# Optimization experiments

Hardware: AMD Instinct MI355X
Metric: run time of the kernel (lower is better)

The kernel has to match this reference:

```python
import jax, jax.numpy as jnp
import numpy as np

EMBED_DIM = 1024
NUM_HEADS = 16
HEAD_DIM = EMBED_DIM // NUM_HEADS


def setup_inputs() -> dict:
    key = jax.random.key(0)
    ks = jax.random.split(key, 7)
    B, S, E = 2, 2048, EMBED_DIM
    s = 1.0 / np.sqrt(E)
    return {
        "x": jax.random.normal(ks[0], (B, S, E), dtype=jnp.float32),
        "W_qkv": jax.random.uniform(ks[1], (3 * E, E), jnp.float32, -s, s),
        "b_qkv": jax.random.uniform(ks[2], (3 * E,), jnp.float32, -s, s),
        "W_proj": jax.random.uniform(ks[3], (E, E), jnp.float32, -s, s),
        "b_proj": jax.random.uniform(ks[4], (E,), jnp.float32, -s, s),
        "gamma": jnp.ones((E,), jnp.float32),
        "beta": jnp.zeros((E,), jnp.float32),
    }


def reference(x, W_qkv, b_qkv, W_proj, b_proj, gamma, beta):
    B, S, E = x.shape
    H, D = NUM_HEADS, HEAD_DIM
    residual = x
    # fused QKV projection: [B,S,3E] -> [B,S,3,H,D]
    qkv = (jnp.einsum('bse,fe->bsf', x, W_qkv) + b_qkv).reshape(B, S, 3, H, D)
    q = qkv[:, :, 0].transpose(0, 2, 1, 3)  # [B,H,S,D]
    k = qkv[:, :, 1].transpose(0, 2, 1, 3)
    v = qkv[:, :, 2].transpose(0, 2, 1, 3)
    scale = 1.0 / jnp.sqrt(jnp.float32(D)).astype(x.dtype)
    attn = jnp.einsum('bhqd,bhkd->bhqk', q, k) * scale  # [B,H,S,S]
    attn = jax.nn.softmax(attn, axis=-1)
    out = jnp.einsum('bhqk,bhkd->bhqd', attn, v)  # [B,H,S,D]
    out = out.transpose(0, 2, 1, 3).reshape(B, S, E)
    out = jnp.einsum('bse,fe->bsf', out, W_proj) + b_proj
    # LayerNorm(out + residual), eps=1e-5 (torch default)
    y = out + residual
    mu = jnp.mean(y, axis=-1, keepdims=True)
    var = jnp.mean(jnp.square(y - mu), axis=-1, keepdims=True)
    return (y - mu) * jax.lax.rsqrt(var + 1e-5) * gamma + beta
```

## Files before the change

kernel.cpp:

```cpp
#include <hip/hip_runtime.h>
#include <cstdint>

#define EDIM 1024
#define NHEADS 16
#define HDIM 64
#define BATCH 2
#define SEQ 2048
#define MROWS (BATCH * SEQ)

typedef __attribute__((ext_vector_type(8))) short bf16x8;
typedef __attribute__((ext_vector_type(4))) float f32x4;

__device__ __forceinline__ unsigned short f2bf(float f) {
  union { float f; unsigned u; } v; v.f = f;
  unsigned r = v.u + 0x7FFFu + ((v.u >> 16) & 1u);
  return (unsigned short)(r >> 16);
}

__device__ __forceinline__ unsigned cvt_pk_bf16(float lo, float hi) {
  unsigned r;
  asm("v_cvt_pk_bf16_f32 %0, %1, %2" : "=v"(r) : "v"(lo), "v"(hi));
  return r;
}

__device__ __forceinline__ void gload16(const void* g, void* l) {
  __builtin_amdgcn_global_load_lds(
      (const __attribute__((address_space(1))) unsigned int*)g,
      (__attribute__((address_space(3))) unsigned int*)l, 16, 0, 0);
}

__global__ __launch_bounds__(256) void cvt_kernel(const float* __restrict__ in,
                                                  unsigned short* __restrict__ out,
                                                  int n) {
  const int i = (blockIdx.x * 256 + threadIdx.x) * 8;
  if (i >= n) return;
  const float4 a = *(const float4*)&in[i];
  const float4 b = *(const float4*)&in[i + 4];
  unsigned short u[8];
  u[0] = f2bf(a.x); u[1] = f2bf(a.y); u[2] = f2bf(a.z); u[3] = f2bf(a.w);
  u[4] = f2bf(b.x); u[5] = f2bf(b.y); u[6] = f2bf(b.z); u[7] = f2bf(b.w);
  *(uint4*)&out[i] = *(uint4*)u;
}

template <int MODE>
__global__ __launch_bounds__(256) void gemm_bf16(
    const unsigned short* __restrict__ A, const unsigned short* __restrict__ Bw,
    const float* __restrict__ bias, const float* __restrict__ resid,
    unsigned short* __restrict__ q_out, unsigned short* __restrict__ k_out,
    unsigned short* __restrict__ v_out, float* __restrict__ y_out,
    int M, int N, int K) {
  __shared__ unsigned short As[128 * 64];
  __shared__ unsigned short Bs[128 * 64];
  const int tid = threadIdx.x;
  const int lane = tid & 63, w = tid >> 6;
  const int wr = w >> 1, wc = w & 1;
  const int l15 = lane & 15, g = lane >> 4;
  const int row0 = blockIdx.y * 128, col0 = blockIdx.x * 128;

  const int er = w * 32 + (lane >> 3);
  const int ec = (lane & 7) * 8;

  f32x4 acc[4][4];
#pragma unroll
  for (int i = 0; i < 4; ++i)
#pragma unroll
    for (int j = 0; j < 4; ++j) acc[i][j] = (f32x4){0.f, 0.f, 0.f, 0.f};

  for (int k0 = 0; k0 < K; k0 += 64) {
    __syncthreads();
#pragma unroll
    for (int t = 0; t < 4; ++t) {
      gload16(&A[(size_t)(row0 + er + t * 8) * K + k0 + ec],
              &As[w * 2048 + t * 512]);
      gload16(&Bw[(size_t)(col0 + er + t * 8) * K + k0 + ec],
              &Bs[w * 2048 + t * 512]);
    }
    __syncthreads();
#pragma unroll
    for (int ks = 0; ks < 2; ++ks) {
      bf16x8 af[4], bfr[4];
#pragma unroll
      for (int i = 0; i < 4; ++i)
        af[i] = *(const bf16x8*)&As[(wr * 64 + i * 16 + l15) * 64 + ks * 32 + g * 8];
#pragma unroll
      for (int j = 0; j < 4; ++j)
        bfr[j] = *(const bf16x8*)&Bs[(wc * 64 + j * 16 + l15) * 64 + ks * 32 + g * 8];
#pragma unroll
      for (int i = 0; i < 4; ++i)
#pragma unroll
        for (int j = 0; j < 4; ++j)
          acc[i][j] = __builtin_amdgcn_mfma_f32_16x16x32_bf16(af[i], bfr[j],
                                                              acc[i][j], 0, 0, 0);
    }
  }

#pragma unroll
  for (int j = 0; j < 4; ++j) {
    const int nbase = col0 + wc * 64 + j * 16 + l15;
    const float bb = bias[nbase];
#pragma unroll
    for (int i = 0; i < 4; ++i) {
#pragma unroll
      for (int r = 0; r < 4; ++r) {
        const int m = row0 + wr * 64 + i * 16 + g * 4 + r;
        float v = acc[i][j][r] + bb;
        if (MODE == 0) {
          const int which = nbase >> 10;
          const int h = (nbase >> 6) & 15, d = nbase & 63;
          const int b = m >> 11, s = m & 2047;
          const size_t idx = ((size_t)(b * NHEADS + h) * SEQ + s) * HDIM + d;
          if (which == 0) q_out[idx] = f2bf(v * 0.125f);
          else if (which == 1) k_out[idx] = f2bf(v);
          else v_out[idx] = f2bf(v);
        } else {
          v += resid[(size_t)m * N + nbase];
          y_out[(size_t)m * N + nbase] = v;
        }
      }
    }
  }
}

__global__ __launch_bounds__(256) void vtrans_kernel(
    const unsigned short* __restrict__ V, unsigned short* __restrict__ Vt) {
  __shared__ unsigned short T[64 * 72];
  const int tid = threadIdx.x;
  const int st = blockIdx.x, bh = blockIdx.y;
  const size_t ibase = (size_t)bh * SEQ * HDIM + (size_t)st * 64 * HDIM;
#pragma unroll
  for (int t = 0; t < 2; ++t) {
    const int chunk = t * 256 + tid;
    const int r = chunk >> 3, c8 = chunk & 7;
    const uint4 v = *(const uint4*)&V[ibase + r * 64 + c8 * 8];
    *(uint4*)&T[r * 72 + c8 * 8] = v;
  }
  __syncthreads();
  const size_t obase = (size_t)bh * HDIM * SEQ + st * 64;
#pragma unroll
  for (int t = 0; t < 2; ++t) {
    const int chunk = t * 256 + tid;
    const int d = chunk >> 3, s8 = (chunk & 7) * 8;
    unsigned short u[8];
#pragma unroll
    for (int e = 0; e < 8; ++e) u[e] = T[(s8 + e) * 72 + d];
    *(uint4*)&Vt[obase + (size_t)d * SEQ + s8] = *(uint4*)u;
  }
}

__global__ __launch_bounds__(512, 4) void attn_mfma(
    const unsigned short* __restrict__ Qb, const unsigned short* __restrict__ Kb,
    const unsigned short* __restrict__ Vt, unsigned short* __restrict__ AO) {
  __shared__ unsigned short K_lds[2][64 * 64];
  __shared__ unsigned short V_lds[2][64 * 64];
  __shared__ unsigned short P_lds[128 * 80];
  const int tid = threadIdx.x;
  const int lane = tid & 63, w = tid >> 6;
  const int l15 = lane & 15, g = lane >> 4;
  const int qt = blockIdx.x;
  const int bh = blockIdx.y;
  const int b = bh >> 4, h = bh & 15;
  const size_t hbase = (size_t)bh * SEQ * HDIM;
  const size_t vbase = (size_t)bh * HDIM * SEQ;
  const int q = qt * 128 + w * 16 + l15;
  const int prow = (w * 16 + l15) * 80;

  const int sr = (w & 3) * 16 + (lane >> 3);
  const int scol = ((lane & 7) ^ (lane >> 3)) * 8;

  bf16x8 aq[2];
#pragma unroll
  for (int ks = 0; ks < 2; ++ks)
    aq[ks] = *(const bf16x8*)&Qb[hbase + (size_t)q * HDIM + ks * 32 + g * 8];

  f32x4 o[4];
#pragma unroll
  for (int jd = 0; jd < 4; ++jd) o[jd] = (f32x4){0.f, 0.f, 0.f, 0.f};
  float mi = -1e30f, li = 0.f;

#define STAGE(buf, kt_)                                                        \
  do {                                                                         \
    if (w < 4) {                                                               \
      gload16(&Kb[hbase + (size_t)((kt_) * 64 + sr) * HDIM + scol],            \
              &K_lds[buf][(w * 16) * 64]);                                     \
      gload16(&Kb[hbase + (size_t)((kt_) * 64 + sr + 8) * HDIM + scol],        \
              &K_lds[buf][(w * 16 + 8) * 64]);                                 \
    } else {                                                                   \
      gload16(&Vt[vbase + (size_t)sr * SEQ + (kt_) * 64 + scol],               \
              &V_lds[buf][((w - 4) * 16) * 64]);                               \
      gload16(&Vt[vbase + (size_t)(sr + 8) * SEQ + (kt_) * 64 + scol],         \
              &V_lds[buf][((w - 4) * 16 + 8) * 64]);                           \
    }                                                                          \
  } while (0)

  STAGE(0, 0);
  for (int kt = 0; kt < SEQ / 64; ++kt) {
    const int cur = kt & 1;
    __syncthreads();
    if (kt + 1 < SEQ / 64) STAGE(cur ^ 1, kt + 1);

    f32x4 scT[4];
#pragma unroll
    for (int j = 0; j < 4; ++j) scT[j] = (f32x4){0.f, 0.f, 0.f, 0.f};
    __builtin_amdgcn_s_setprio(1);
#pragma unroll
    for (int ks = 0; ks < 2; ++ks) {
      bf16x8 bk[4];
#pragma unroll
      for (int j = 0; j < 4; ++j)
        bk[j] = *(const bf16x8*)&K_lds[cur][(j * 16 + l15) * 64 +
                                            (((ks * 4 + g) ^ (l15 & 7)) * 8)];
#pragma unroll
      for (int j = 0; j < 4; ++j)
        scT[j] = __builtin_amdgcn_mfma_f32_16x16x32_bf16(bk[j], aq[ks],
                                                         scT[j], 0, 0, 0);
    }
    __builtin_amdgcn_s_setprio(0);

    float tm = scT[0][0];
#pragma unroll
    for (int j = 0; j < 4; ++j)
#pragma unroll
      for (int r = 0; r < 4; ++r) tm = fmaxf(tm, scT[j][r]);
    tm = fmaxf(tm, __shfl_xor(tm, 16));
    tm = fmaxf(tm, __shfl_xor(tm, 32));
    const float mn = fmaxf(mi, tm);
    const float al = __expf(mi - mn);
    mi = mn;
    float p[4][4];
    float rs = 0.f;
#pragma unroll
    for (int j = 0; j < 4; ++j)
#pragma unroll
      for (int r = 0; r < 4; ++r) {
        p[j][r] = __expf(scT[j][r] - mn);
        rs += p[j][r];
      }
    rs += __shfl_xor(rs, 16);
    rs += __shfl_xor(rs, 32);
    li = li * al + rs;
#pragma unroll
    for (int j = 0; j < 4; ++j) {
      *(unsigned*)&P_lds[prow + j * 16 + g * 4 + 0] = cvt_pk_bf16(p[j][0], p[j][1]);
      *(unsigned*)&P_lds[prow + j * 16 + g * 4 + 2] = cvt_pk_bf16(p[j][2], p[j][3]);
    }
#pragma unroll
    for (int jd = 0; jd < 4; ++jd)
#pragma unroll
      for (int r = 0; r < 4; ++r) o[jd][r] *= al;

    __builtin_amdgcn_s_setprio(1);
#pragma unroll
    for (int ks = 0; ks < 2; ++ks) {
      const bf16x8 ap = *(const bf16x8*)&P_lds[prow + ks * 32 + g * 8];
      bf16x8 bv[4];
#pragma unroll
      for (int jd = 0; jd < 4; ++jd)
        bv[jd] = *(const bf16x8*)&V_lds[cur][(jd * 16 + l15) * 64 +
                                             (((ks * 4 + g) ^ (l15 & 7)) * 8)];
#pragma unroll
      for (int jd = 0; jd < 4; ++jd)
        o[jd] = __builtin_amdgcn_mfma_f32_16x16x32_bf16(bv[jd], ap, o[jd], 0, 0, 0);
    }
    __builtin_amdgcn_s_setprio(0);
  }
#undef STAGE

  const float inv = 1.f / li;
#pragma unroll
  for (int jd = 0; jd < 4; ++jd) {
    uint2 u;
    u.x = cvt_pk_bf16(o[jd][0] * inv, o[jd][1] * inv);
    u.y = cvt_pk_bf16(o[jd][2] * inv, o[jd][3] * inv);
    *(uint2*)&AO[(size_t)(b * SEQ + q) * EDIM + h * HDIM + jd * 16 + g * 4] = u;
  }
}

__global__ __launch_bounds__(256) void ln_kernel(float* __restrict__ y,
                                                 const float* __restrict__ gamma,
                                                 const float* __restrict__ beta) {
  const int row = blockIdx.x, tid = threadIdx.x;
  const float4 v = *reinterpret_cast<const float4*>(&y[(size_t)row * EDIM + tid * 4]);
  float s = v.x + v.y + v.z + v.w;
  float s2 = v.x * v.x + v.y * v.y + v.z * v.z + v.w * v.w;
#pragma unroll
  for (int off = 1; off < 64; off <<= 1) {
    s += __shfl_xor(s, off);
    s2 += __shfl_xor(s2, off);
  }
  __shared__ float red[8];
  if ((tid & 63) == 0) {
    red[(tid >> 6) * 2 + 0] = s;
    red[(tid >> 6) * 2 + 1] = s2;
  }
  __syncthreads();
  s = red[0] + red[2] + red[4] + red[6];
  s2 = red[1] + red[3] + red[5] + red[7];
  const float mean = s * (1.f / 1024.f);
  const float var = fmaxf(s2 * (1.f / 1024.f) - mean * mean, 0.f);
  const float rstd = rsqrtf(var + 1e-5f);
  const float4 gm = *reinterpret_cast<const float4*>(&gamma[tid * 4]);
  const float4 be = *reinterpret_cast<const float4*>(&beta[tid * 4]);
  float4 outv;
  outv.x = (v.x - mean) * rstd * gm.x + be.x;
  outv.y = (v.y - mean) * rstd * gm.y + be.y;
  outv.z = (v.z - mean) * rstd * gm.z + be.z;
  outv.w = (v.w - mean) * rstd * gm.w + be.w;
  *reinterpret_cast<float4*>(&y[(size_t)row * EDIM + tid * 4]) = outv;
}

extern "C" void kernel_launch(void* const* d_in, const int* in_sizes, int n_in,
                              void* d_out, int out_size, void* d_ws,
                              size_t ws_size, hipStream_t stream) {
  const float* x = (const float*)d_in[0];
  const float* W_qkv = (const float*)d_in[1];
  const float* b_qkv = (const float*)d_in[2];
  const float* W_proj = (const float*)d_in[3];
  const float* b_proj = (const float*)d_in[4];
  const float* gamma = (const float*)d_in[5];
  const float* beta = (const float*)d_in[6];
  float* out = (float*)d_out;

  uint8_t* p = (uint8_t*)d_ws;
  unsigned short* x_bf = (unsigned short*)p;            p += (size_t)MROWS * EDIM * 2;
  unsigned short* wqkv_bf = (unsigned short*)p;         p += (size_t)3 * EDIM * EDIM * 2;
  unsigned short* wproj_bf = (unsigned short*)p;        p += (size_t)EDIM * EDIM * 2;
  unsigned short* Qb = (unsigned short*)p;              p += (size_t)MROWS * EDIM * 2;
  unsigned short* Kb = (unsigned short*)p;              p += (size_t)MROWS * EDIM * 2;
  unsigned short* Vb = (unsigned short*)p;              p += (size_t)MROWS * EDIM * 2;
  unsigned short* Vtb = (unsigned short*)p;             p += (size_t)MROWS * EDIM * 2;
  unsigned short* AOb = (unsigned short*)p;             p += (size_t)MROWS * EDIM * 2;

  cvt_kernel<<<(MROWS * EDIM / 8 + 255) / 256, 256, 0, stream>>>(x, x_bf, MROWS * EDIM);
  cvt_kernel<<<(3 * EDIM * EDIM / 8 + 255) / 256, 256, 0, stream>>>(W_qkv, wqkv_bf, 3 * EDIM * EDIM);
  cvt_kernel<<<(EDIM * EDIM / 8 + 255) / 256, 256, 0, stream>>>(W_proj, wproj_bf, EDIM * EDIM);

  gemm_bf16<0><<<dim3(24, 32), 256, 0, stream>>>(x_bf, wqkv_bf, b_qkv, nullptr,
                                                 Qb, Kb, Vb, nullptr,
                                                 MROWS, 3 * EDIM, EDIM);
  vtrans_kernel<<<dim3(SEQ / 64, BATCH * NHEADS), 256, 0, stream>>>(Vb, Vtb);
  attn_mfma<<<dim3(SEQ / 128, BATCH * NHEADS), 512, 0, stream>>>(Qb, Kb, Vtb, AOb);
  gemm_bf16<1><<<dim3(8, 32), 256, 0, stream>>>(AOb, wproj_bf, b_proj, x,
                                                nullptr, nullptr, nullptr, out,
                                                MROWS, EDIM, EDIM);
  ln_kernel<<<MROWS, 256, 0, stream>>>(out, gamma, beta);
}
```

Measured before the change: 246.0 us.

## Fuse conversion kernels, remap GEMM blocks, use exp2 softmax with deferred rescale

Merges the three fp32-to-bf16 conversion launches into one kernel that uses packed hardware conversion. Remaps GEMM block indices so consecutive workgroups share weight tiles, which should improve L2 reuse. In attention, folds log2(e) into the Q scale so softmax can use exp2, and skips the running-max rescale of the output accumulator unless the new max exceeds the old one by more than 8. It also replaces the padded P buffer with an XOR-swizzled layout to avoid LDS bank conflicts. The deferred rescale relies on fp32 headroom, since unnormalized exponentials can reach 2^8 before a rescale happens.

```diff
diff --git a/kernel.cpp b/kernel.cpp
--- a/kernel.cpp
+++ b/kernel.cpp
@@ -11,6 +11,8 @@
 typedef __attribute__((ext_vector_type(8))) short bf16x8;
 typedef __attribute__((ext_vector_type(4))) float f32x4;
 
+#define QSCALE 0.18033688011112042f
+
 __device__ __forceinline__ unsigned short f2bf(float f) {
   union { float f; unsigned u; } v; v.f = f;
   unsigned r = v.u + 0x7FFFu + ((v.u >> 16) & 1u);
@@ -29,17 +31,31 @@
       (__attribute__((address_space(3))) unsigned int*)l, 16, 0, 0);
 }
 
-__global__ __launch_bounds__(256) void cvt_kernel(const float* __restrict__ in,
-                                                  unsigned short* __restrict__ out,
-                                                  int n) {
-  const int i = (blockIdx.x * 256 + threadIdx.x) * 8;
-  if (i >= n) return;
-  const float4 a = *(const float4*)&in[i];
-  const float4 b = *(const float4*)&in[i + 4];
-  unsigned short u[8];
-  u[0] = f2bf(a.x); u[1] = f2bf(a.y); u[2] = f2bf(a.z); u[3] = f2bf(a.w);
-  u[4] = f2bf(b.x); u[5] = f2bf(b.y); u[6] = f2bf(b.z); u[7] = f2bf(b.w);
-  *(uint4*)&out[i] = *(uint4*)u;
+__global__ __launch_bounds__(256) void cvt_all_kernel(
+    const float* __restrict__ x, const float* __restrict__ wq,
+    const float* __restrict__ wp, unsigned short* __restrict__ xo,
+    unsigned short* __restrict__ wqo, unsigned short* __restrict__ wpo) {
+  const int NX = MROWS * EDIM, NQ = 3 * EDIM * EDIM, NP = EDIM * EDIM;
+  int i = (blockIdx.x * 256 + threadIdx.x) * 8;
+  const float* src;
+  unsigned short* dst;
+  if (i < NX) {
+    src = x + i; dst = xo + i;
+  } else if (i < NX + NQ) {
+    src = wq + (i - NX); dst = wqo + (i - NX);
+  } else if (i < NX + NQ + NP) {
+    src = wp + (i - NX - NQ); dst = wpo + (i - NX - NQ);
+  } else {
+    return;
+  }
+  const float4 a = *(const float4*)&src[0];
+  const float4 b = *(const float4*)&src[4];
+  unsigned u[4];
+  u[0] = cvt_pk_bf16(a.x, a.y);
+  u[1] = cvt_pk_bf16(a.z, a.w);
+  u[2] = cvt_pk_bf16(b.x, b.y);
+  u[3] = cvt_pk_bf16(b.z, b.w);
+  *(uint4*)dst = *(uint4*)u;
 }
 
 template <int MODE>
@@ -55,7 +71,13 @@
   const int lane = tid & 63, w = tid >> 6;
   const int wr = w >> 1, wc = w & 1;
   const int l15 = lane & 15, g = lane >> 4;
-  const int row0 = blockIdx.y * 128, col0 = blockIdx.x * 128;
+
+  const int flat = blockIdx.y * gridDim.x + blockIdx.x;
+  const int xk = flat & 7, xi = flat >> 3;
+  int bx, by;
+  if (MODE == 0) { bx = xk * 3 + (xi >> 5); by = xi & 31; }
+  else           { bx = xk;                 by = xi; }
+  const int row0 = by * 128, col0 = bx * 128;
 
   const int er = w * 32 + (lane >> 3);
   const int ec = (lane & 7) * 8;
@@ -109,7 +131,7 @@
           const int h = (nbase >> 6) & 15, d = nbase & 63;
           const int b = m >> 11, s = m & 2047;
           const size_t idx = ((size_t)(b * NHEADS + h) * SEQ + s) * HDIM + d;
-          if (which == 0) q_out[idx] = f2bf(v * 0.125f);
+          if (which == 0) q_out[idx] = f2bf(v * QSCALE);
           else if (which == 1) k_out[idx] = f2bf(v);
           else v_out[idx] = f2bf(v);
         } else {
@@ -152,7 +174,7 @@
     const unsigned short* __restrict__ Vt, unsigned short* __restrict__ AO) {
   __shared__ unsigned short K_lds[2][64 * 64];
   __shared__ unsigned short V_lds[2][64 * 64];
-  __shared__ unsigned short P_lds[128 * 80];
+  __shared__ unsigned P32[128 * 32];
   const int tid = threadIdx.x;
   const int lane = tid & 63, w = tid >> 6;
   const int l15 = lane & 15, g = lane >> 4;
@@ -162,7 +184,7 @@
   const size_t hbase = (size_t)bh * SEQ * HDIM;
   const size_t vbase = (size_t)bh * HDIM * SEQ;
   const int q = qt * 128 + w * 16 + l15;
-  const int prow = (w * 16 + l15) * 80;
+  const int prow32 = (w * 16 + l15) * 32;
 
   const int sr = (w & 3) * 16 + (lane >> 3);
   const int scol = ((lane & 7) ^ (lane >> 3)) * 8;
@@ -223,35 +245,46 @@
       for (int r = 0; r < 4; ++r) tm = fmaxf(tm, scT[j][r]);
     tm = fmaxf(tm, __shfl_xor(tm, 16));
     tm = fmaxf(tm, __shfl_xor(tm, 32));
-    const float mn = fmaxf(mi, tm);
-    const float al = __expf(mi - mn);
-    mi = mn;
+    const bool defer = __all(tm <= mi + 8.f) != 0;
+    float al = 1.f;
+    if (!defer) {
+      const float mn = fmaxf(mi, tm);
+      al = exp2f(mi - mn);
+      mi = mn;
+#pragma unroll
+      for (int jd = 0; jd < 4; ++jd)
+#pragma unroll
+        for (int r = 0; r < 4; ++r) o[jd][r] *= al;
+    }
     float p[4][4];
     float rs = 0.f;
 #pragma unroll
     for (int j = 0; j < 4; ++j)
 #pragma unroll
       for (int r = 0; r < 4; ++r) {
-        p[j][r] = __expf(scT[j][r] - mn);
+        p[j][r] = exp2f(scT[j][r] - mi);
         rs += p[j][r];
       }
     rs += __shfl_xor(rs, 16);
     rs += __shfl_xor(rs, 32);
     li = li * al + rs;
+
 #pragma unroll
     for (int j = 0; j < 4; ++j) {
-      *(unsigned*)&P_lds[prow + j * 16 + g * 4 + 0] = cvt_pk_bf16(p[j][0], p[j][1]);
-      *(unsigned*)&P_lds[prow + j * 16 + g * 4 + 2] = cvt_pk_bf16(p[j][2], p[j][3]);
-    }
-#pragma unroll
-    for (int jd = 0; jd < 4; ++jd)
-#pragma unroll
-      for (int r = 0; r < 4; ++r) o[jd][r] *= al;
+      const unsigned u01 = cvt_pk_bf16(p[j][0], p[j][1]);
+      const unsigned u23 = cvt_pk_bf16(p[j][2], p[j][3]);
+      const int c = (j * 4 + g) ^ l15;
+      *(uint2*)&P32[prow32 + c * 2] = make_uint2(u01, u23);
+    }
 
     __builtin_amdgcn_s_setprio(1);
 #pragma unroll
     for (int ks = 0; ks < 2; ++ks) {
-      const bf16x8 ap = *(const bf16x8*)&P_lds[prow + ks * 32 + g * 8];
+      const int cb = ks * 8 + g * 2;
+      const uint2 a0 = *(const uint2*)&P32[prow32 + ((cb) ^ l15) * 2];
+      const uint2 a1 = *(const uint2*)&P32[prow32 + ((cb + 1) ^ l15) * 2];
+      unsigned pa[4] = {a0.x, a0.y, a1.x, a1.y};
+      const bf16x8 ap = *(const bf16x8*)pa;
       bf16x8 bv[4];
 #pragma unroll
       for (int jd = 0; jd < 4; ++jd)
@@ -330,9 +363,9 @@
   unsigned short* Vtb = (unsigned short*)p;             p += (size_t)MROWS * EDIM * 2;
   unsigned short* AOb = (unsigned short*)p;             p += (size_t)MROWS * EDIM * 2;
 
-  cvt_kernel<<<(MROWS * EDIM / 8 + 255) / 256, 256, 0, stream>>>(x, x_bf, MROWS * EDIM);
-  cvt_kernel<<<(3 * EDIM * EDIM / 8 + 255) / 256, 256, 0, stream>>>(W_qkv, wqkv_bf, 3 * EDIM * EDIM);
-  cvt_kernel<<<(EDIM * EDIM / 8 + 255) / 256, 256, 0, stream>>>(W_proj, wproj_bf, EDIM * EDIM);
+  const int NCVT = MROWS * EDIM + 3 * EDIM * EDIM + EDIM * EDIM;
+  cvt_all_kernel<<<(NCVT / 8 + 255) / 256, 256, 0, stream>>>(
+      x, W_qkv, W_proj, x_bf, wqkv_bf, wproj_bf);
 
   gemm_bf16<0><<<dim3(24, 32), 256, 0, stream>>>(x_bf, wqkv_bf, b_qkv, nullptr,
                                                  Qb, Kb, Vb, nullptr,
```

Measured after the change: 248.3 us. Within noise of the previous version (+0.9%).
